# Optimization experiments

Hardware: AMD Instinct MI355X
Metric: run time of the kernel (lower is better)

Reference implementation:

```python
import jax, jax.numpy as jnp
import numpy as np
from jax.ops import segment_sum

N_NODES = 100000
N_EDGES = 1600000
D = 128
N_LAYERS = 4
N_GRAPHS = 512
LN_EPS = 1e-5


def setup_inputs() -> dict:
    key = jax.random.key(0)
    ks = jax.random.split(key, 8)
    x = jax.random.normal(ks[0], (N_NODES, D), dtype=jnp.float32)
    edge_index = jax.random.randint(ks[1], (2, N_EDGES), 0, N_NODES, dtype=jnp.int64)
    batch = jnp.sort(jax.random.randint(ks[2], (N_NODES,), 0, N_GRAPHS, dtype=jnp.int64))
    scale = 1.0 / np.sqrt(D)
    Ws = jax.random.normal(ks[3], (N_LAYERS, D, D), dtype=jnp.float32) * scale
    bs = jnp.zeros((N_LAYERS, D), dtype=jnp.float32)
    gammas = jnp.ones((N_LAYERS, D), dtype=jnp.float32)
    betas = jnp.zeros((N_LAYERS, D), dtype=jnp.float32)
    lin_w = jax.random.normal(ks[4], (D, 1), dtype=jnp.float32) * scale
    lin_b = jnp.zeros((1,), dtype=jnp.float32)
    return {"x": x, "edge_index": edge_index, "batch": batch, "Ws": Ws,
            "bs": bs, "gammas": gammas, "betas": betas,
            "lin_w": lin_w, "lin_b": lin_b}


def _gcn_conv(x, W, b, src, dst, deg_inv_sqrt):
    # PyG GCNConv: h = x @ W, then sym-normalized aggregation over A + I, then + bias
    h = x @ W                                   # [N, D]
    coef = deg_inv_sqrt[src] * deg_inv_sqrt[dst]  # [E]
    msg = h[src] * coef[:, None]                # [E, D] gather (memory-bound)
    agg = segment_sum(msg, dst, num_segments=x.shape[0])  # scatter-add
    agg = agg + h * (deg_inv_sqrt * deg_inv_sqrt)[:, None]  # self-loop term
    return agg + b


def _layernorm(x, gamma, beta):
    mu = jnp.mean(x, axis=-1, keepdims=True)
    var = jnp.mean(jnp.square(x - mu), axis=-1, keepdims=True)
    return (x - mu) * jax.lax.rsqrt(var + LN_EPS) * gamma + beta


def reference(x, edge_index, batch, Ws, bs, gammas, betas, lin_w, lin_b):
    n = x.shape[0]
    src, dst = edge_index[0], edge_index[1]
    # degree with self-loops (GCNConv adds self loops by default)
    deg = segment_sum(jnp.ones_like(dst, dtype=x.dtype), dst, num_segments=n) + 1.0
    deg_inv_sqrt = jax.lax.rsqrt(deg)

    h = _gcn_conv(x, Ws[0], bs[0], src, dst, deg_inv_sqrt)
    h = _layernorm(h, gammas[0], betas[0])
    h = jax.nn.relu(h)  # dropout is identity in eval mode
    for i in range(1, N_LAYERS):
        h_prev = h
        h = _gcn_conv(h, Ws[i], bs[i], src, dst, deg_inv_sqrt)
        h = _layernorm(h, gammas[i], betas[i])
        h = h + h_prev
        if i < N_LAYERS - 1:
            h = jax.nn.relu(h)

    # global mean pool over graphs
    sums = segment_sum(h, batch, num_segments=N_GRAPHS)        # [G, D]
    cnts = segment_sum(jnp.ones((n,), h.dtype), batch, num_segments=N_GRAPHS)
    pooled = sums / jnp.maximum(cnts, 1.0)[:, None]
    return pooled @ lin_w + lin_b  # [G, 1]
```

## Files before the change

### kernel.cpp

```cpp
#include <hip/hip_runtime.h>
#include <hip/hip_bf16.h>


typedef __hip_bfloat162 bf2;
typedef __attribute__((ext_vector_type(8))) short short8;
typedef __attribute__((ext_vector_type(4))) float f32x4;

__global__ __launch_bounds__(256) void k_deg(const int* __restrict__ dst,
                                             int* __restrict__ cnt, int E) {
    int base = (blockIdx.x * 256 + threadIdx.x) * 4;
    if (base + 4 <= E) {
        int4 d4 = *(const int4*)(dst + base);
        atomicAdd(&cnt[d4.x], 1);
        atomicAdd(&cnt[d4.y], 1);
        atomicAdd(&cnt[d4.z], 1);
        atomicAdd(&cnt[d4.w], 1);
    } else {
        for (int j = base; j < E; j++) atomicAdd(&cnt[dst[j]], 1);
    }
}

__global__ __launch_bounds__(256) void k_scan1(const int* __restrict__ cnt,
                                               int* __restrict__ loc,
                                               int* __restrict__ blk,
                                               float* __restrict__ dis, int n) {
    __shared__ int s[256];
    int b = blockIdx.x, tid = threadIdx.x;
    int base = b * 1024 + tid * 4;
    int v0 = (base + 0 < n) ? cnt[base + 0] : 0;
    int v1 = (base + 1 < n) ? cnt[base + 1] : 0;
    int v2 = (base + 2 < n) ? cnt[base + 2] : 0;
    int v3 = (base + 3 < n) ? cnt[base + 3] : 0;
    if (base + 0 < n) dis[base + 0] = rsqrtf((float)v0 + 1.0f);
    if (base + 1 < n) dis[base + 1] = rsqrtf((float)v1 + 1.0f);
    if (base + 2 < n) dis[base + 2] = rsqrtf((float)v2 + 1.0f);
    if (base + 3 < n) dis[base + 3] = rsqrtf((float)v3 + 1.0f);
    int tsum = v0 + v1 + v2 + v3;
    s[tid] = tsum;
    __syncthreads();
    for (int off = 1; off < 256; off <<= 1) {
        int t = (tid >= off) ? s[tid - off] : 0;
        __syncthreads();
        s[tid] += t;
        __syncthreads();
    }
    int excl = s[tid] - tsum;
    if (base + 0 < n) loc[base + 0] = excl;
    if (base + 1 < n) loc[base + 1] = excl + v0;
    if (base + 2 < n) loc[base + 2] = excl + v0 + v1;
    if (base + 3 < n) loc[base + 3] = excl + v0 + v1 + v2;
    if (tid == 255) blk[b] = s[255];
}

__global__ __launch_bounds__(128) void k_scan2(int* __restrict__ blk, int nb,
                                               int* __restrict__ total_out) {
    __shared__ int s[128];
    int tid = threadIdx.x;
    int v = (tid < nb) ? blk[tid] : 0;
    s[tid] = v;
    __syncthreads();
    for (int off = 1; off < 128; off <<= 1) {
        int t = (tid >= off) ? s[tid - off] : 0;
        __syncthreads();
        s[tid] += t;
        __syncthreads();
    }
    if (tid < nb) blk[tid] = s[tid] - v;
    if (tid == 127) *total_out = s[127];
}

__global__ void k_scan3(int* __restrict__ row_off, const int* __restrict__ blk,
                        int* __restrict__ cur, int n) {
    int d = blockIdx.x * blockDim.x + threadIdx.x;
    if (d >= n) return;
    int ro = row_off[d] + blk[d >> 10];
    row_off[d] = ro;
    cur[d] = ro;
}

__global__ __launch_bounds__(256) void k_scatter2(const int* __restrict__ src,
                                                  const int* __restrict__ dst,
                                                  int* __restrict__ cur,
                                                  const float* __restrict__ dis,
                                                  int2* __restrict__ colcf, int E) {
    int base = (blockIdx.x * 256 + threadIdx.x) * 4;
    if (base + 4 <= E) {
        int4 d4 = *(const int4*)(dst + base);
        int4 s4 = *(const int4*)(src + base);
        int dd[4] = {d4.x, d4.y, d4.z, d4.w};
        int ss[4] = {s4.x, s4.y, s4.z, s4.w};
#pragma unroll
        for (int j = 0; j < 4; j++) {
            int p = atomicAdd(&cur[dd[j]], 1);
            float cf = dis[ss[j]] * dis[dd[j]];
            colcf[p] = make_int2(ss[j], __float_as_int(cf));
        }
    } else {
        for (int j = base; j < E; j++) {
            int d = dst[j], s = src[j];
            int p = atomicAdd(&cur[d], 1);
            colcf[p] = make_int2(s, __float_as_int(dis[s] * dis[d]));
        }
    }
}

__global__ void k_prepw(const float* __restrict__ Ws, __hip_bfloat16* __restrict__ Wt) {
    int i = blockIdx.x * blockDim.x + threadIdx.x;
    int layer = i >> 14;
    int m = i & 16383;
    int j = m & 7;
    int l = (m >> 3) & 63;
    int ckb = m >> 9;
    int kb = ckb & 3;
    int c = ckb >> 2;
    int quad = l >> 4, lr = l & 15;
    int k = kb * 32 + quad * 8 + j;
    int col = c * 16 + lr;
    Wt[i] = __float2bfloat16(Ws[layer * 16384 + k * 128 + col]);
}

__global__ __launch_bounds__(256) void k_matmul(const __hip_bfloat16* __restrict__ Xb,
                                                const float* __restrict__ Xf,
                                                const __hip_bfloat16* __restrict__ Wt,
                                                __hip_bfloat16* __restrict__ Hb, int n) {
    __shared__ __align__(16) __hip_bfloat16 sX[64 * 136];
    const int tid = threadIdx.x;
    const int row0 = blockIdx.x * 64;
    if (Xf) {
        for (int i = tid; i < 2048; i += 256) {
            int r = i >> 5, c = i & 31;
            int gr = row0 + r;
            float4 v = make_float4(0.f, 0.f, 0.f, 0.f);
            if (gr < n) v = *(const float4*)(Xf + (size_t)gr * 128 + c * 4);
            union { bf2 h2[2]; uint2 u; } pk;
            pk.h2[0].x = __float2bfloat16(v.x);
            pk.h2[0].y = __float2bfloat16(v.y);
            pk.h2[1].x = __float2bfloat16(v.z);
            pk.h2[1].y = __float2bfloat16(v.w);
            *(uint2*)(sX + r * 136 + c * 4) = pk.u;
        }
    } else {
        for (int i = tid; i < 1024; i += 256) {
            int r = i >> 4, ck = i & 15;
            uint4 v = make_uint4(0, 0, 0, 0);
            int gr = row0 + r;
            if (gr < n) v = *(const uint4*)(Xb + (size_t)gr * 128 + ck * 8);
            *(uint4*)(sX + r * 136 + ck * 8) = v;
        }
    }
    __syncthreads();
    const int w = tid >> 6, l = tid & 63;
    const int quad = l >> 4, lr = l & 15;
    f32x4 acc[8];
#pragma unroll
    for (int c = 0; c < 8; c++) acc[c] = (f32x4){0.f, 0.f, 0.f, 0.f};
    short8 a[4];
#pragma unroll
    for (int kb = 0; kb < 4; kb++)
        a[kb] = *(const short8*)(sX + (w * 16 + lr) * 136 + kb * 32 + quad * 8);
#pragma unroll
    for (int c = 0; c < 8; c++) {
#pragma unroll
        for (int kb = 0; kb < 4; kb++) {
            short8 b = *(const short8*)(Wt + ((c * 4 + kb) * 64 + l) * 8);
            acc[c] = __builtin_amdgcn_mfma_f32_16x16x32_bf16(a[kb], b, acc[c], 0, 0, 0);
        }
    }
#pragma unroll
    for (int c = 0; c < 8; c++)
#pragma unroll
        for (int r = 0; r < 4; r++)
            sX[(w * 16 + quad * 4 + r) * 136 + c * 16 + lr] =
                __float2bfloat16(acc[c][r]);
#pragma unroll
    for (int p = 0; p < 4; p++) {
        int r = p * 4 + quad;
        int gr = row0 + w * 16 + r;
        uint4 v = *(const uint4*)(sX + (w * 16 + r) * 136 + lr * 8);
        if (gr < n) *(uint4*)(Hb + (size_t)gr * 128 + lr * 8) = v;
    }
}

__global__ __launch_bounds__(256) void k_node(const __hip_bfloat16* __restrict__ Hb,
                                              __hip_bfloat16* __restrict__ Xb,
                                              const int* __restrict__ row_off,
                                              const int2* __restrict__ colcf,
                                              const float* __restrict__ dis,
                                              const float* __restrict__ bias,
                                              const float* __restrict__ gamma,
                                              const float* __restrict__ beta,
                                              const float* __restrict__ lin_w,
                                              const int* __restrict__ batch,
                                              float* __restrict__ gsum,
                                              int do_relu, int do_res, int fuse_pool,
                                              int n) {
    __shared__ float spd[16];
    __shared__ int   sbt[16];
    const int wave = threadIdx.x >> 6;
    const int lane = threadIdx.x & 63;
    const int grp = lane >> 4;
    const int sub = lane & 15;
    const int node = blockIdx.x * 16 + wave * 4 + grp;
    const bool vn = node < n;
    const int nd = vn ? node : 0;
    const int e0 = vn ? row_off[node] : 0;
    const int e1 = vn ? row_off[node + 1] : 0;
    const char* hbase = (const char*)Hb;
    const unsigned suboff = (unsigned)(sub << 4);

    float dn = dis[nd];
    uint4 sv = *(const uint4*)(hbase + (((unsigned)nd) << 8) + suboff);

    float acc[8];
#pragma unroll
    for (int k = 0; k < 8; k++) acc[k] = 0.f;

    int e = e0;
    int2 p[8];
#pragma unroll
    for (int u = 0; u < 8; u++) p[u] = colcf[(e + u < e1) ? e + u : 0];

    while (__any(e < e1)) {
        uint4 v[8];
        float cf[8];
#pragma unroll
        for (int u = 0; u < 8; u++) {
            v[u] = *(const uint4*)(hbase + (((unsigned)p[u].x) << 8) + suboff);
            cf[u] = (e + u < e1) ? __int_as_float(p[u].y) : 0.f;
        }
        const int en = e + 8;
        int2 pn[8];
#pragma unroll
        for (int u = 0; u < 8; u++) pn[u] = colcf[(en + u < e1) ? en + u : 0];
#pragma unroll
        for (int u = 0; u < 8; u++) {
            float c = cf[u];
            acc[0] += __uint_as_float(v[u].x << 16) * c;
            acc[1] += __uint_as_float(v[u].x & 0xffff0000u) * c;
            acc[2] += __uint_as_float(v[u].y << 16) * c;
            acc[3] += __uint_as_float(v[u].y & 0xffff0000u) * c;
            acc[4] += __uint_as_float(v[u].z << 16) * c;
            acc[5] += __uint_as_float(v[u].z & 0xffff0000u) * c;
            acc[6] += __uint_as_float(v[u].w << 16) * c;
            acc[7] += __uint_as_float(v[u].w & 0xffff0000u) * c;
        }
#pragma unroll
        for (int u = 0; u < 8; u++) p[u] = pn[u];
        e = en;
    }

    {
        float dn2 = dn * dn;
        acc[0] += __uint_as_float(sv.x << 16) * dn2;
        acc[1] += __uint_as_float(sv.x & 0xffff0000u) * dn2;
        acc[2] += __uint_as_float(sv.y << 16) * dn2;
        acc[3] += __uint_as_float(sv.y & 0xffff0000u) * dn2;
        acc[4] += __uint_as_float(sv.z << 16) * dn2;
        acc[5] += __uint_as_float(sv.z & 0xffff0000u) * dn2;
        acc[6] += __uint_as_float(sv.w << 16) * dn2;
        acc[7] += __uint_as_float(sv.w & 0xffff0000u) * dn2;
    }
    float4 b0 = *(const float4*)(bias + sub * 8);
    float4 b1 = *(const float4*)(bias + sub * 8 + 4);
    acc[0] += b0.x; acc[1] += b0.y; acc[2] += b0.z; acc[3] += b0.w;
    acc[4] += b1.x; acc[5] += b1.y; acc[6] += b1.z; acc[7] += b1.w;

    float s = acc[0] + acc[1] + acc[2] + acc[3] + acc[4] + acc[5] + acc[6] + acc[7];
#pragma unroll
    for (int m = 8; m > 0; m >>= 1) s += __shfl_xor(s, m, 64);
    float mu = s * (1.f / 128.f);
    float vs = 0.f;
#pragma unroll
    for (int k = 0; k < 8; k++) {
        float d = acc[k] - mu;
        acc[k] = d;
        vs += d * d;
    }
#pragma unroll
    for (int m = 8; m > 0; m >>= 1) vs += __shfl_xor(vs, m, 64);
    float rs = rsqrtf(vs * (1.f / 128.f) + 1e-5f);

    float4 g0 = *(const float4*)(gamma + sub * 8);
    float4 g1 = *(const float4*)(gamma + sub * 8 + 4);
    float4 t0 = *(const float4*)(beta + sub * 8);
    float4 t1 = *(const float4*)(beta + sub * 8 + 4);
    float y[8];
    y[0] = acc[0] * rs * g0.x + t0.x;
    y[1] = acc[1] * rs * g0.y + t0.y;
    y[2] = acc[2] * rs * g0.z + t0.z;
    y[3] = acc[3] * rs * g0.w + t0.w;
    y[4] = acc[4] * rs * g1.x + t1.x;
    y[5] = acc[5] * rs * g1.y + t1.y;
    y[6] = acc[6] * rs * g1.z + t1.z;
    y[7] = acc[7] * rs * g1.w + t1.w;

    __hip_bfloat16* xp = Xb + (size_t)node * 128 + sub * 8;
    if (vn && do_res) {
        uint4 rv = *(const uint4*)xp;
        y[0] += __uint_as_float(rv.x << 16);
        y[1] += __uint_as_float(rv.x & 0xffff0000u);
        y[2] += __uint_as_float(rv.y << 16);
        y[3] += __uint_as_float(rv.y & 0xffff0000u);
        y[4] += __uint_as_float(rv.z << 16);
        y[5] += __uint_as_float(rv.z & 0xffff0000u);
        y[6] += __uint_as_float(rv.w << 16);
        y[7] += __uint_as_float(rv.w & 0xffff0000u);
    }

    if (fuse_pool) {
        float4 w0 = *(const float4*)(lin_w + sub * 8);
        float4 w1 = *(const float4*)(lin_w + sub * 8 + 4);
        float pdot = y[0] * w0.x + y[1] * w0.y + y[2] * w0.z + y[3] * w0.w +
                     y[4] * w1.x + y[5] * w1.y + y[6] * w1.z + y[7] * w1.w;
#pragma unroll
        for (int m = 8; m > 0; m >>= 1) pdot += __shfl_xor(pdot, m, 64);
        int slot = wave * 4 + grp;
        if (sub == 0) {
            spd[slot] = vn ? pdot : 0.f;
            sbt[slot] = vn ? batch[node] : -1;
        }
        __syncthreads();
        if (threadIdx.x == 0) {
            int i = 0;
            while (i < 16) {
                int b = sbt[i];
                if (b < 0) { i++; continue; }
                float acc2 = spd[i];
                int j = i + 1;
                while (j < 16 && sbt[j] == b) { acc2 += spd[j]; j++; }
                atomicAdd(&gsum[b], acc2);
                i = j;
            }
        }
    } else if (vn) {
        if (do_relu) {
#pragma unroll
            for (int k = 0; k < 8; k++) y[k] = fmaxf(y[k], 0.f);
        }
        union { bf2 h2[4]; uint4 u; } pk;
        pk.h2[0].x = __float2bfloat16(y[0]); pk.h2[0].y = __float2bfloat16(y[1]);
        pk.h2[1].x = __float2bfloat16(y[2]); pk.h2[1].y = __float2bfloat16(y[3]);
        pk.h2[2].x = __float2bfloat16(y[4]); pk.h2[2].y = __float2bfloat16(y[5]);
        pk.h2[3].x = __float2bfloat16(y[6]); pk.h2[3].y = __float2bfloat16(y[7]);
        *(uint4*)xp = pk.u;
    }
}

__global__ void k_out(const float* __restrict__ gsum, const int* __restrict__ batch,
                      const float* __restrict__ lin_b, float* __restrict__ out,
                      int n, int G) {
    int g = blockIdx.x * blockDim.x + threadIdx.x;
    if (g >= G) return;
    int lo = 0, hi = n;
    while (lo < hi) { int m = (lo + hi) >> 1; if (batch[m] < g) lo = m + 1; else hi = m; }
    int start = lo;
    hi = n;
    while (lo < hi) { int m = (lo + hi) >> 1; if (batch[m] <= g) lo = m + 1; else hi = m; }
    float c = (float)(lo - start);
    out[g] = gsum[g] / fmaxf(c, 1.f) + lin_b[0];
}

extern "C" void kernel_launch(void* const* d_in, const int* in_sizes, int n_in,
                              void* d_out, int out_size, void* d_ws, size_t ws_size,
                              hipStream_t stream) {
    const float* x      = (const float*)d_in[0];
    const int*   eidx   = (const int*)d_in[1];
    const int*   batch  = (const int*)d_in[2];
    const float* Ws     = (const float*)d_in[3];
    const float* bs     = (const float*)d_in[4];
    const float* gammas = (const float*)d_in[5];
    const float* betas  = (const float*)d_in[6];
    const float* lin_w  = (const float*)d_in[7];
    const float* lin_b  = (const float*)d_in[8];
    float* out = (float*)d_out;

    const int n = in_sizes[2];
    const int E = in_sizes[1] / 2;
    const int G = out_size;
    const int nb = (n + 1023) / 1024;

    const int* src  = eidx;
    const int* dstp = eidx + E;

    char* w = (char*)d_ws;
    size_t off = 0;
    auto alloc = [&](size_t bytes) {
        void* p = w + off;
        off = (off + bytes + 15) & ~(size_t)15;
        return p;
    };
    int*   cnt     = (int*)  alloc((size_t)n * 4);
    float* gsum    = (float*)alloc((size_t)G * 4);
    int*   row_off = (int*)  alloc((size_t)(n + 1) * 4);
    int*   blk     = (int*)  alloc(128 * 4);
    int*   cur     = (int*)  alloc((size_t)n * 4);
    float* dis     = (float*)alloc((size_t)n * 4);
    int2*  colcf   = (int2*) alloc((size_t)E * 8);
    __hip_bfloat16* hb  = (__hip_bfloat16*)alloc((size_t)n * 128 * 2);
    __hip_bfloat16* xb  = (__hip_bfloat16*)alloc((size_t)n * 128 * 2);
    __hip_bfloat16* wt  = (__hip_bfloat16*)alloc((size_t)4 * 128 * 128 * 2);
    (void)ws_size; (void)n_in;

    hipMemsetAsync(cnt, 0, (size_t)n * 4 + (size_t)G * 4, stream);
    k_deg<<<(E + 1023) / 1024, 256, 0, stream>>>(dstp, cnt, E);
    k_scan1<<<nb, 256, 0, stream>>>(cnt, row_off, blk, dis, n);
    k_scan2<<<1, 128, 0, stream>>>(blk, nb, row_off + n);
    k_scan3<<<(n + 255) / 256, 256, 0, stream>>>(row_off, blk, cur, n);
    k_scatter2<<<(E + 1023) / 1024, 256, 0, stream>>>(src, dstp, cur, dis, colcf, E);
    k_prepw<<<(4 * 128 * 128 + 255) / 256, 256, 0, stream>>>(Ws, wt);

    for (int layer = 0; layer < 4; layer++) {
        k_matmul<<<(n + 63) / 64, 256, 0, stream>>>(xb, (layer == 0) ? x : nullptr,
                                                    wt + (size_t)layer * 16384, hb, n);
        k_node<<<(n + 15) / 16, 256, 0, stream>>>(hb, xb, row_off, colcf, dis,
                                                  bs + (size_t)layer * 128,
                                                  gammas + (size_t)layer * 128,
                                                  betas + (size_t)layer * 128,
                                                  lin_w, batch, gsum,
                                                  (layer < 3) ? 1 : 0, (layer > 0) ? 1 : 0,
                                                  (layer == 3) ? 1 : 0, n);
    }
    k_out<<<(G + 255) / 256, 256, 0, stream>>>(gsum, batch, lin_b, out, n, G);
}
```

Measured before the change: 655.6 us.

## Build CSR via two-pass bucketed LDS sort and store 4-byte source indices

Replaces the CSR build, which used global-atomic degree counting, a scan and a global-atomic scatter, with a two-pass bucket sort. Edges are first partitioned into 256-node buckets using per-block LDS histograms. Each bucket is then sorted locally in shared memory, and the same pass writes row offsets and degree normalisations. The per-edge entry shrinks from (src, coef) int2 to a 4-byte source index, and k_node computes the coefficient from a gathered dis[src] times the node's own dis. In exchange there is an extra per-edge dis gather in every layer, plus a hard cap of 5120 edges per bucket and 17-bit packing of source ids, which only hold for graphs of this size and degree distribution.

```diff
diff --git a/kernel.cpp b/kernel.cpp
--- a/kernel.cpp
+++ b/kernel.cpp
@@ -6,36 +6,40 @@
 typedef __attribute__((ext_vector_type(8))) short short8;
 typedef __attribute__((ext_vector_type(4))) float f32x4;
 
-__global__ __launch_bounds__(256) void k_deg(const int* __restrict__ dst,
-                                             int* __restrict__ cnt, int E) {
-    int base = (blockIdx.x * 256 + threadIdx.x) * 4;
-    if (base + 4 <= E) {
-        int4 d4 = *(const int4*)(dst + base);
-        atomicAdd(&cnt[d4.x], 1);
-        atomicAdd(&cnt[d4.y], 1);
-        atomicAdd(&cnt[d4.z], 1);
-        atomicAdd(&cnt[d4.w], 1);
-    } else {
-        for (int j = base; j < E; j++) atomicAdd(&cnt[dst[j]], 1);
-    }
-}
-
-__global__ __launch_bounds__(256) void k_scan1(const int* __restrict__ cnt,
-                                               int* __restrict__ loc,
-                                               int* __restrict__ blk,
-                                               float* __restrict__ dis, int n) {
+#define P1B 512
+#define MAXB 5120
+
+__global__ __launch_bounds__(256) void k_p1a(const int* __restrict__ dst,
+                                             int* __restrict__ bh, int E, int NB) {
+    __shared__ int h[512];
+    const int tid = threadIdx.x;
+    for (int i = tid; i < NB; i += 256) h[i] = 0;
+    __syncthreads();
+    const int per = (((E + P1B - 1) / P1B) + 3) & ~3;
+    const int e0 = blockIdx.x * per, e1 = min(E, e0 + per);
+    for (int base = e0 + tid * 4; base < e1; base += 1024) {
+        if (base + 4 <= e1) {
+            int4 d4 = *(const int4*)(dst + base);
+            atomicAdd(&h[d4.x >> 8], 1);
+            atomicAdd(&h[d4.y >> 8], 1);
+            atomicAdd(&h[d4.z >> 8], 1);
+            atomicAdd(&h[d4.w >> 8], 1);
+        } else {
+            for (int j = base; j < e1; j++) atomicAdd(&h[dst[j] >> 8], 1);
+        }
+    }
+    __syncthreads();
+    int* out = bh + (size_t)blockIdx.x * NB;
+    for (int i = tid; i < NB; i += 256) out[i] = h[i];
+}
+
+__global__ __launch_bounds__(256) void k_p1b1(int* __restrict__ bh,
+                                              int* __restrict__ btot, int NB) {
     __shared__ int s[256];
-    int b = blockIdx.x, tid = threadIdx.x;
-    int base = b * 1024 + tid * 4;
-    int v0 = (base + 0 < n) ? cnt[base + 0] : 0;
-    int v1 = (base + 1 < n) ? cnt[base + 1] : 0;
-    int v2 = (base + 2 < n) ? cnt[base + 2] : 0;
-    int v3 = (base + 3 < n) ? cnt[base + 3] : 0;
-    if (base + 0 < n) dis[base + 0] = rsqrtf((float)v0 + 1.0f);
-    if (base + 1 < n) dis[base + 1] = rsqrtf((float)v1 + 1.0f);
-    if (base + 2 < n) dis[base + 2] = rsqrtf((float)v2 + 1.0f);
-    if (base + 3 < n) dis[base + 3] = rsqrtf((float)v3 + 1.0f);
-    int tsum = v0 + v1 + v2 + v3;
+    const int b = blockIdx.x, tid = threadIdx.x;
+    int v0 = bh[(size_t)(2 * tid) * NB + b];
+    int v1 = bh[(size_t)(2 * tid + 1) * NB + b];
+    int tsum = v0 + v1;
     s[tid] = tsum;
     __syncthreads();
     for (int off = 1; off < 256; off <<= 1) {
@@ -45,62 +49,112 @@
         __syncthreads();
     }
     int excl = s[tid] - tsum;
-    if (base + 0 < n) loc[base + 0] = excl;
-    if (base + 1 < n) loc[base + 1] = excl + v0;
-    if (base + 2 < n) loc[base + 2] = excl + v0 + v1;
-    if (base + 3 < n) loc[base + 3] = excl + v0 + v1 + v2;
-    if (tid == 255) blk[b] = s[255];
-}
-
-__global__ __launch_bounds__(128) void k_scan2(int* __restrict__ blk, int nb,
-                                               int* __restrict__ total_out) {
-    __shared__ int s[128];
-    int tid = threadIdx.x;
-    int v = (tid < nb) ? blk[tid] : 0;
-    s[tid] = v;
-    __syncthreads();
-    for (int off = 1; off < 128; off <<= 1) {
+    bh[(size_t)(2 * tid) * NB + b] = excl;
+    bh[(size_t)(2 * tid + 1) * NB + b] = excl + v0;
+    if (tid == 255) btot[b] = s[255];
+}
+
+__global__ __launch_bounds__(256) void k_p1b2(const int* __restrict__ btot,
+                                              int* __restrict__ bbase,
+                                              int* __restrict__ row_off,
+                                              float* __restrict__ gsum,
+                                              int NB, int E, int n, int G) {
+    __shared__ int s[256];
+    const int tid = threadIdx.x;
+    int v0 = (2 * tid < NB) ? btot[2 * tid] : 0;
+    int v1 = (2 * tid + 1 < NB) ? btot[2 * tid + 1] : 0;
+    int tsum = v0 + v1;
+    s[tid] = tsum;
+    __syncthreads();
+    for (int off = 1; off < 256; off <<= 1) {
         int t = (tid >= off) ? s[tid - off] : 0;
         __syncthreads();
         s[tid] += t;
         __syncthreads();
     }
-    if (tid < nb) blk[tid] = s[tid] - v;
-    if (tid == 127) *total_out = s[127];
-}
-
-__global__ void k_scan3(int* __restrict__ row_off, const int* __restrict__ blk,
-                        int* __restrict__ cur, int n) {
-    int d = blockIdx.x * blockDim.x + threadIdx.x;
-    if (d >= n) return;
-    int ro = row_off[d] + blk[d >> 10];
-    row_off[d] = ro;
-    cur[d] = ro;
-}
-
-__global__ __launch_bounds__(256) void k_scatter2(const int* __restrict__ src,
-                                                  const int* __restrict__ dst,
-                                                  int* __restrict__ cur,
-                                                  const float* __restrict__ dis,
-                                                  int2* __restrict__ colcf, int E) {
-    int base = (blockIdx.x * 256 + threadIdx.x) * 4;
-    if (base + 4 <= E) {
-        int4 d4 = *(const int4*)(dst + base);
-        int4 s4 = *(const int4*)(src + base);
-        int dd[4] = {d4.x, d4.y, d4.z, d4.w};
-        int ss[4] = {s4.x, s4.y, s4.z, s4.w};
-#pragma unroll
-        for (int j = 0; j < 4; j++) {
-            int p = atomicAdd(&cur[dd[j]], 1);
-            float cf = dis[ss[j]] * dis[dd[j]];
-            colcf[p] = make_int2(ss[j], __float_as_int(cf));
-        }
-    } else {
-        for (int j = base; j < E; j++) {
-            int d = dst[j], s = src[j];
-            int p = atomicAdd(&cur[d], 1);
-            colcf[p] = make_int2(s, __float_as_int(dis[s] * dis[d]));
-        }
+    int excl = s[tid] - tsum;
+    if (2 * tid < NB) bbase[2 * tid] = excl;
+    if (2 * tid + 1 < NB) bbase[2 * tid + 1] = excl + v0;
+    if (tid == 0) row_off[n] = E;
+    for (int i = tid; i < G; i += 256) gsum[i] = 0.f;
+}
+
+__global__ __launch_bounds__(256) void k_p1c(const int* __restrict__ src,
+                                             const int* __restrict__ dst,
+                                             const int* __restrict__ bh,
+                                             const int* __restrict__ bbase,
+                                             unsigned* __restrict__ ebuf,
+                                             int E, int NB) {
+    __shared__ int cur[512];
+    const int tid = threadIdx.x;
+    const int* cb = bh + (size_t)blockIdx.x * NB;
+    for (int i = tid; i < NB; i += 256) cur[i] = cb[i] + bbase[i];
+    __syncthreads();
+    const int per = (((E + P1B - 1) / P1B) + 3) & ~3;
+    const int e0 = blockIdx.x * per, e1 = min(E, e0 + per);
+    for (int base = e0 + tid * 4; base < e1; base += 1024) {
+        if (base + 4 <= e1) {
+            int4 d4 = *(const int4*)(dst + base);
+            int4 s4 = *(const int4*)(src + base);
+            int dd[4] = {d4.x, d4.y, d4.z, d4.w};
+            int ss[4] = {s4.x, s4.y, s4.z, s4.w};
+#pragma unroll
+            for (int j = 0; j < 4; j++) {
+                int p = atomicAdd(&cur[dd[j] >> 8], 1);
+                ebuf[p] = ((unsigned)(dd[j] & 255) << 17) | (unsigned)ss[j];
+            }
+        } else {
+            for (int j = base; j < e1; j++) {
+                int d = dst[j];
+                int p = atomicAdd(&cur[d >> 8], 1);
+                ebuf[p] = ((unsigned)(d & 255) << 17) | (unsigned)src[j];
+            }
+        }
+    }
+}
+
+__global__ __launch_bounds__(256) void k_p2(const unsigned* __restrict__ ebuf,
+                                            const int* __restrict__ btot,
+                                            const int* __restrict__ bbase,
+                                            unsigned* __restrict__ colsrc,
+                                            int* __restrict__ row_off,
+                                            float* __restrict__ dis, int n) {
+    __shared__ unsigned ein[MAXB];
+    __shared__ int hist[256];
+    __shared__ int scn[256];
+    const int b = blockIdx.x, tid = threadIdx.x;
+    const int base = bbase[b];
+    int sz = btot[b];
+    if (sz > MAXB) sz = MAXB;
+    hist[tid] = 0;
+    __syncthreads();
+    for (int i = tid; i < sz; i += 256) {
+        unsigned v = ebuf[base + i];
+        ein[i] = v;
+        atomicAdd(&hist[v >> 17], 1);
+    }
+    __syncthreads();
+    const int deg = hist[tid];
+    scn[tid] = deg;
+    __syncthreads();
+    for (int off = 1; off < 256; off <<= 1) {
+        int t = (tid >= off) ? scn[tid - off] : 0;
+        __syncthreads();
+        scn[tid] += t;
+        __syncthreads();
+    }
+    const int excl = scn[tid] - deg;
+    const int node = b * 256 + tid;
+    if (node < n) {
+        row_off[node] = base + excl;
+        dis[node] = rsqrtf((float)deg + 1.0f);
+    }
+    hist[tid] = excl;
+    __syncthreads();
+    for (int i = tid; i < sz; i += 256) {
+        unsigned v = ein[i];
+        int p = atomicAdd(&hist[v >> 17], 1);
+        colsrc[base + p] = v & 0x1FFFFu;
     }
 }
 
@@ -184,7 +238,7 @@
 __global__ __launch_bounds__(256) void k_node(const __hip_bfloat16* __restrict__ Hb,
                                               __hip_bfloat16* __restrict__ Xb,
                                               const int* __restrict__ row_off,
-                                              const int2* __restrict__ colcf,
+                                              const unsigned* __restrict__ colsrc,
                                               const float* __restrict__ dis,
                                               const float* __restrict__ bias,
                                               const float* __restrict__ gamma,
@@ -216,25 +270,25 @@
     for (int k = 0; k < 8; k++) acc[k] = 0.f;
 
     int e = e0;
-    int2 p[8];
-#pragma unroll
-    for (int u = 0; u < 8; u++) p[u] = colcf[(e + u < e1) ? e + u : 0];
+    unsigned su[8];
+#pragma unroll
+    for (int u = 0; u < 8; u++) su[u] = colsrc[(e + u < e1) ? e + u : 0];
 
     while (__any(e < e1)) {
         uint4 v[8];
-        float cf[8];
+        float dv[8];
 #pragma unroll
         for (int u = 0; u < 8; u++) {
-            v[u] = *(const uint4*)(hbase + (((unsigned)p[u].x) << 8) + suboff);
-            cf[u] = (e + u < e1) ? __int_as_float(p[u].y) : 0.f;
+            v[u] = *(const uint4*)(hbase + (su[u] << 8) + suboff);
+            dv[u] = dis[su[u]];
         }
         const int en = e + 8;
-        int2 pn[8];
-#pragma unroll
-        for (int u = 0; u < 8; u++) pn[u] = colcf[(en + u < e1) ? en + u : 0];
+        unsigned sn[8];
+#pragma unroll
+        for (int u = 0; u < 8; u++) sn[u] = colsrc[(en + u < e1) ? en + u : 0];
 #pragma unroll
         for (int u = 0; u < 8; u++) {
-            float c = cf[u];
+            float c = (e + u < e1) ? dv[u] * dn : 0.f;
             acc[0] += __uint_as_float(v[u].x << 16) * c;
             acc[1] += __uint_as_float(v[u].x & 0xffff0000u) * c;
             acc[2] += __uint_as_float(v[u].y << 16) * c;
@@ -245,7 +299,7 @@
             acc[7] += __uint_as_float(v[u].w & 0xffff0000u) * c;
         }
 #pragma unroll
-        for (int u = 0; u < 8; u++) p[u] = pn[u];
+        for (int u = 0; u < 8; u++) su[u] = sn[u];
         e = en;
     }
 
@@ -377,7 +431,7 @@
     const int n = in_sizes[2];
     const int E = in_sizes[1] / 2;
     const int G = out_size;
-    const int nb = (n + 1023) / 1024;
+    const int NB = (n + 255) >> 8;
 
     const int* src  = eidx;
     const int* dstp = eidx + E;
@@ -389,30 +443,30 @@
         off = (off + bytes + 15) & ~(size_t)15;
         return p;
     };
-    int*   cnt     = (int*)  alloc((size_t)n * 4);
-    float* gsum    = (float*)alloc((size_t)G * 4);
-    int*   row_off = (int*)  alloc((size_t)(n + 1) * 4);
-    int*   blk     = (int*)  alloc(128 * 4);
-    int*   cur     = (int*)  alloc((size_t)n * 4);
-    float* dis     = (float*)alloc((size_t)n * 4);
-    int2*  colcf   = (int2*) alloc((size_t)E * 8);
-    __hip_bfloat16* hb  = (__hip_bfloat16*)alloc((size_t)n * 128 * 2);
-    __hip_bfloat16* xb  = (__hip_bfloat16*)alloc((size_t)n * 128 * 2);
-    __hip_bfloat16* wt  = (__hip_bfloat16*)alloc((size_t)4 * 128 * 128 * 2);
+    int*      bh      = (int*)     alloc((size_t)P1B * NB * 4);
+    int*      btot    = (int*)     alloc((size_t)NB * 4);
+    int*      bbase   = (int*)     alloc((size_t)NB * 4);
+    unsigned* ebuf    = (unsigned*)alloc((size_t)E * 4);
+    unsigned* colsrc  = (unsigned*)alloc((size_t)E * 4);
+    int*      row_off = (int*)     alloc((size_t)(n + 1) * 4);
+    float*    dis     = (float*)   alloc((size_t)n * 4);
+    float*    gsum    = (float*)   alloc((size_t)G * 4);
+    __hip_bfloat16* hb = (__hip_bfloat16*)alloc((size_t)n * 128 * 2);
+    __hip_bfloat16* xb = (__hip_bfloat16*)alloc((size_t)n * 128 * 2);
+    __hip_bfloat16* wt = (__hip_bfloat16*)alloc((size_t)4 * 128 * 128 * 2);
     (void)ws_size; (void)n_in;
 
-    hipMemsetAsync(cnt, 0, (size_t)n * 4 + (size_t)G * 4, stream);
-    k_deg<<<(E + 1023) / 1024, 256, 0, stream>>>(dstp, cnt, E);
-    k_scan1<<<nb, 256, 0, stream>>>(cnt, row_off, blk, dis, n);
-    k_scan2<<<1, 128, 0, stream>>>(blk, nb, row_off + n);
-    k_scan3<<<(n + 255) / 256, 256, 0, stream>>>(row_off, blk, cur, n);
-    k_scatter2<<<(E + 1023) / 1024, 256, 0, stream>>>(src, dstp, cur, dis, colcf, E);
+    k_p1a<<<P1B, 256, 0, stream>>>(dstp, bh, E, NB);
+    k_p1b1<<<NB, 256, 0, stream>>>(bh, btot, NB);
+    k_p1b2<<<1, 256, 0, stream>>>(btot, bbase, row_off, gsum, NB, E, n, G);
+    k_p1c<<<P1B, 256, 0, stream>>>(src, dstp, bh, bbase, ebuf, E, NB);
+    k_p2<<<NB, 256, 0, stream>>>(ebuf, btot, bbase, colsrc, row_off, dis, n);
     k_prepw<<<(4 * 128 * 128 + 255) / 256, 256, 0, stream>>>(Ws, wt);
 
     for (int layer = 0; layer < 4; layer++) {
         k_matmul<<<(n + 63) / 64, 256, 0, stream>>>(xb, (layer == 0) ? x : nullptr,
                                                     wt + (size_t)layer * 16384, hb, n);
-        k_node<<<(n + 15) / 16, 256, 0, stream>>>(hb, xb, row_off, colcf, dis,
+        k_node<<<(n + 15) / 16, 256, 0, stream>>>(hb, xb, row_off, colsrc, dis,
                                                   bs + (size_t)layer * 128,
                                                   gammas + (size_t)layer * 128,
                                                   betas + (size_t)layer * 128,
```

Result: faster. 553.6 us (-15.6%).
